# Kernel tuning notes

Measured on AMD Instinct MI355X. Metric: run time of the kernel, lower is better.

The kernel has to match this reference:

```python
import jax, jax.numpy as jnp
import numpy as np

H = 32          # heads
E = 32          # head dim = mdl_channels // heads (must equal heads per module bug)
C = 1024        # mdl_channels == in_channels
MAXP = 128      # max_position_embeddings
EPS = 1e-5


def _layernorm(x, g, b):
    mu = jnp.mean(x, axis=-1, keepdims=True)
    var = jnp.var(x, axis=-1, keepdims=True)
    return (x - mu) * jax.lax.rsqrt(var + EPS) * g + b


def setup_inputs() -> dict:
    key = jax.random.key(0)
    ks = jax.random.split(key, 16)
    s = 0.02
    N, L = 4, 1024
    inp = {
        "x": jax.random.normal(ks[0], (N, L, C), jnp.float32),
        "Wq": jax.random.normal(ks[1], (C, C), jnp.float32) * s,
        "bq": jnp.zeros((C,), jnp.float32),
        "Wk": jax.random.normal(ks[2], (C, C), jnp.float32) * s,
        "bk": jnp.zeros((C,), jnp.float32),
        "Wv": jax.random.normal(ks[3], (C, C), jnp.float32) * s,
        "bv": jnp.zeros((C,), jnp.float32),
        "dist_emb": jax.random.normal(ks[4], (2 * MAXP + 1, E), jnp.float32) * s,
        "ln1_g": jnp.ones((C,), jnp.float32),
        "ln1_b": jnp.zeros((C,), jnp.float32),
        "ln2_g": jnp.ones((C,), jnp.float32),
        "ln2_b": jnp.zeros((C,), jnp.float32),
        "W1": jax.random.normal(ks[5], (C, C), jnp.float32) * s,
        "b1": jnp.zeros((C,), jnp.float32),
        "W2": jax.random.normal(ks[6], (C, C), jnp.float32) * s,
        "b2": jnp.zeros((C,), jnp.float32),
    }
    return inp


def reference(x, Wq, bq, Wk, bk, Wv, bv, dist_emb, ln1_g, ln1_b,
              ln2_g, ln2_b, W1, b1, W2, b2):
    N, L, _ = x.shape
    # QKV projections -> (N, L, H, E)
    q = (x @ Wq + bq).reshape(N, L, H, E)
    k = (x @ Wk + bk).reshape(N, L, H, E)
    v = (x @ Wv + bv).reshape(N, L, H, E)

    temp = 1.0 / np.sqrt(E).astype(np.float32)
    # content scores (N, H, L, S)
    QK = jnp.einsum('nlhe,nshe->nhls', q, k)
    # relative position scores (disentangled attention)
    pos = jnp.arange(L)
    dist = jnp.clip(pos[:, None] - pos[None, :], -MAXP, MAXP) + MAXP  # (L, L)
    pe = dist_emb[dist]                                              # (L, L, E)
    QK = QK + jnp.einsum('nlhe,lse->nhls', q, pe) \
            + jnp.einsum('nshe,lse->nhls', k, pe)
    A = jax.nn.softmax(temp * QK, axis=-1)          # dropout: eval mode (identity)
    t = jnp.einsum('nhls,nshe->nlhe', A, v).reshape(N, L, C)

    h = _layernorm(t + x, ln1_g, ln1_b)             # AddNorm (attention)
    m = jax.nn.relu(h @ W1 + b1) @ W2 + b2          # 2-layer MLP
    out = _layernorm(m + h, ln2_g, ln2_b)           # AddNorm (mlp)
    return jnp.swapaxes(out, 0, 1)                  # 'n f c -> f n c'
```

## Files before the change

kernel.cpp:

```cpp
#include <hip/hip_runtime.h>

#define H_ 32
#define E_ 32
#define C_ 1024
#define L_ 1024
#define N_ 4
#define M_ 4096
#define NH_ 128
#define D_ 257
#define QDP 264
#define TEMP_ 0.17677669529663687f

typedef unsigned short u16;
typedef __attribute__((ext_vector_type(8))) short short8;
typedef __attribute__((ext_vector_type(4))) float f32x4;
typedef __attribute__((ext_vector_type(4))) unsigned short u16x4;

__device__ __forceinline__ u16 f2bf(float f) {
  union { float f; unsigned u; } v; v.f = f;
  unsigned r = v.u + 0x7fffu + ((v.u >> 16) & 1u);
  return (u16)(r >> 16);
}
__device__ __forceinline__ float bf2f(u16 h) {
  union { unsigned u; float f; } v; v.u = ((unsigned)h) << 16;
  return v.f;
}
__device__ __forceinline__ f32x4 mfma16(short8 a, short8 b, f32x4 c) {
  return __builtin_amdgcn_mfma_f32_16x16x32_bf16(a, b, c, 0, 0, 0);
}

__global__ __launch_bounds__(256) void prep_kernel(
    const float* __restrict__ demb, const float* __restrict__ bq,
    const float* __restrict__ bk, const float* __restrict__ bv,
    u16* __restrict__ demb_b, float* __restrict__ bqkv) {
  int i = blockIdx.x * 256 + threadIdx.x;
  if (i < D_ * E_) demb_b[i] = f2bf(demb[i]);
  if (i < C_) { bqkv[i] = bq[i]; bqkv[C_ + i] = bk[i]; bqkv[2 * C_ + i] = bv[i]; }
}

__global__ __launch_bounds__(256) void cvt_x_kernel(const float* __restrict__ x,
                                                    u16* __restrict__ xb) {
  int i = blockIdx.x * 256 + threadIdx.x;
  f32x4 v = reinterpret_cast<const f32x4*>(x)[i];
  u16x4 o2;
  o2[0] = f2bf(v[0]); o2[1] = f2bf(v[1]); o2[2] = f2bf(v[2]); o2[3] = f2bf(v[3]);
  reinterpret_cast<u16x4*>(xb)[i] = o2;
}

__global__ __launch_bounds__(256) void transpose_w_kernel(const float* __restrict__ in,
                                                          u16* __restrict__ out) {
  __shared__ float tile[32][33];
  int j0 = blockIdx.x * 32, c0 = blockIdx.y * 32;
#pragma unroll
  for (int i = 0; i < 4; ++i) {
    int cy = threadIdx.y + i * 8;
    tile[cy][threadIdx.x] = in[(size_t)(c0 + cy) * C_ + j0 + threadIdx.x];
  }
  __syncthreads();
#pragma unroll
  for (int i = 0; i < 4; ++i) {
    int jy = threadIdx.y + i * 8;
    out[(size_t)(j0 + jy) * C_ + c0 + threadIdx.x] = f2bf(tile[threadIdx.x][jy]);
  }
}

template <int EPI>
__global__ __launch_bounds__(256) void gemm128_kernel(
    const u16* __restrict__ A, const u16* __restrict__ Bt, int K,
    const float* __restrict__ bias,
    u16* __restrict__ out0, u16* __restrict__ out1, u16* __restrict__ out2) {
  __shared__ u16 As[128 * 64];
  __shared__ u16 Bs[128 * 64];
  const int bid = blockIdx.x;
  const int m0 = (bid & 31) << 7;
  const int n0 = (bid >> 5) << 7;
  const int tid = threadIdx.x;
  const int w = tid >> 6, lane = tid & 63, lhi = lane >> 4, llo = lane & 15;
  const int wr = w >> 1, wc = w & 1;
  f32x4 acc[4][4] = {};
  for (int k0 = 0; k0 < K; k0 += 64) {
#pragma unroll
    for (int i = 0; i < 4; ++i) {
      int e = i * 256 + tid;
      int row = e >> 3, c8 = (e & 7) << 3;
      *reinterpret_cast<short8*>(&As[row * 64 + c8]) =
          *reinterpret_cast<const short8*>(&A[(size_t)(m0 + row) * K + k0 + c8]);
      *reinterpret_cast<short8*>(&Bs[row * 64 + c8]) =
          *reinterpret_cast<const short8*>(&Bt[(size_t)(n0 + row) * K + k0 + c8]);
    }
    __syncthreads();
#pragma unroll
    for (int kk = 0; kk < 2; ++kk) {
      const int ko = (kk << 5) + lhi * 8;
      short8 af[4], bf[4];
#pragma unroll
      for (int mi = 0; mi < 4; ++mi)
        af[mi] = *reinterpret_cast<const short8*>(&As[(wr * 64 + mi * 16 + llo) * 64 + ko]);
#pragma unroll
      for (int ni = 0; ni < 4; ++ni)
        bf[ni] = *reinterpret_cast<const short8*>(&Bs[(wc * 64 + ni * 16 + llo) * 64 + ko]);
#pragma unroll
      for (int mi = 0; mi < 4; ++mi)
#pragma unroll
        for (int ni = 0; ni < 4; ++ni)
          acc[mi][ni] = mfma16(af[mi], bf[ni], acc[mi][ni]);
    }
    __syncthreads();
  }
#pragma unroll
  for (int mi = 0; mi < 4; ++mi)
#pragma unroll
    for (int ni = 0; ni < 4; ++ni)
#pragma unroll
      for (int r = 0; r < 4; ++r) {
        int row = m0 + wr * 64 + mi * 16 + lhi * 4 + r;
        int col = n0 + wc * 64 + ni * 16 + llo;
        float v = acc[mi][ni][r] + bias[col];
        if constexpr (EPI == 0) {
          int which = col >> 10, jj = col & 1023, h = jj >> 5, e2 = jj & 31;
          int n = row >> 10, l = row & 1023;
          int nh = (n << 5) | h;
          if (which == 0) v *= TEMP_;
          u16 bvv = f2bf(v);
          if (which == 0)      out0[((size_t)((nh << 10) | l)) * 32 + e2] = bvv;
          else if (which == 1) out1[((size_t)((nh << 10) | l)) * 32 + e2] = bvv;
          else                 out2[(((size_t)(nh * 32 + e2)) << 10) | l] = bvv;
        } else if constexpr (EPI == 1) {
          out0[(size_t)row * C_ + col] = f2bf(fmaxf(v, 0.f));
        } else {
          out0[(size_t)row * C_ + col] = f2bf(v);
        }
      }
}

__global__ __launch_bounds__(256) void qdkd_kernel(
    const u16* __restrict__ src, const u16* __restrict__ demb,
    u16* __restrict__ dst, int dstride, float scale,
    u16* __restrict__ aux0, u16* __restrict__ aux256) {
  const int wt = blockIdx.x * 4 + (threadIdx.x >> 6);
  const int lane = threadIdx.x & 63, lhi = lane >> 4, llo = lane & 15;
  const int m0 = wt << 4;
  short8 a = *reinterpret_cast<const short8*>(&src[(size_t)(m0 + llo) * E_ + lhi * 8]);
#pragma unroll
  for (int ct = 0; ct < 17; ++ct) {
    int d = ct * 16 + llo;
    short8 b = {0, 0, 0, 0, 0, 0, 0, 0};
    if (d < D_) b = *reinterpret_cast<const short8*>(&demb[d * E_ + lhi * 8]);
    f32x4 c = {};
    c = mfma16(a, b, c);
    if (d < D_) {
#pragma unroll
      for (int r = 0; r < 4; ++r) {
        u16 val = f2bf(c[r] * scale);
        dst[(size_t)(m0 + lhi * 4 + r) * dstride + d] = val;
        if (aux0 != nullptr && d == 0)     aux0[m0 + lhi * 4 + r] = val;
        if (aux256 != nullptr && d == 256) aux256[m0 + lhi * 4 + r] = val;
      }
    }
  }
}

__global__ __launch_bounds__(256) void attn_kernel(
    const u16* __restrict__ qw, const u16* __restrict__ kw,
    const u16* __restrict__ vT, const u16* __restrict__ QDg,
    const u16* __restrict__ KDg, const u16* __restrict__ kd0a,
    const u16* __restrict__ kd256a, u16* __restrict__ tb) {
  __shared__ u16 QDs[64 * QDP];
  __shared__ u16 kdc[2 * 1024];
  __shared__ u16 Pbuf[4 * 512];
  const int bid = blockIdx.x;
  const int nh = bid >> 4;
  const int l0 = (bid & 15) << 6;
  const int tid = threadIdx.x;
  const int w = tid >> 6, lane = tid & 63, lhi = lane >> 4, llo = lane & 15;
  const int lw0 = l0 + (w << 4);
  const int lg = lw0 + llo;
  const int lrow = (w << 4) + llo;

  const u16* qb  = qw + (size_t)nh * (L_ * E_);
  const u16* kb  = kw + (size_t)nh * (L_ * E_);
  const u16* vb  = vT + (size_t)nh * (E_ * L_);
  const u16* qdg = QDg + (size_t)nh * ((size_t)L_ * QDP);
  const u16* kdg = KDg + (size_t)nh * ((size_t)L_ * D_);

  {
    const int rr = tid >> 5, cc = tid & 31;
#pragma unroll
    for (int g = 0; g < 8; ++g) {
      int row = g * 8 + rr;
      *reinterpret_cast<short8*>(&QDs[row * QDP + cc * 8]) =
          *reinterpret_cast<const short8*>(&qdg[(size_t)(l0 + row) * QDP + cc * 8]);
    }
    if (tid < 64) QDs[tid * QDP + 256] = qdg[(size_t)(l0 + tid) * QDP + 256];
    const int side = tid >> 7, off = (tid & 127) * 8;
    const u16* srcA = (side ? kd256a : kd0a) + (size_t)nh * L_ + off;
    *reinterpret_cast<short8*>(&kdc[side * 1024 + off]) =
        *reinterpret_cast<const short8*>(srcA);
  }
  __syncthreads();

  const short8 qB = *reinterpret_cast<const short8*>(&qb[(size_t)lg * E_ + lhi * 8]);
  const float qd0   = bf2f(QDs[lrow * QDP + 0]);
  const float qd256 = bf2f(QDs[lrow * QDP + 256]);

  f32x4 o0 = {}, o1 = {};
  float l_acc = 0.f;
  char* Pw = reinterpret_cast<char*>(&Pbuf[w * 512]);

  for (int s0 = 0; s0 < L_; s0 += 32) {
    short8 kA0 = *reinterpret_cast<const short8*>(&kb[(size_t)(s0 + llo) * E_ + lhi * 8]);
    short8 kA1 = *reinterpret_cast<const short8*>(&kb[(size_t)(s0 + 16 + llo) * E_ + lhi * 8]);
    f32x4 st0 = {}, st1 = {};
    st0 = mfma16(kA0, qB, st0);
    st1 = mfma16(kA1, qB, st1);

    float p[8];
    const bool far_hi = (lw0 - (s0 + 31)) >= 128;
    const bool far_lo = (s0 - (lw0 + 15)) >= 128;
    if (far_hi || far_lo) {
      const float qdc = far_hi ? qd256 : qd0;
      const u16* kcb = &kdc[far_hi ? 1024 : 0];
      u16x4 kc0 = *reinterpret_cast<const u16x4*>(&kcb[s0 + lhi * 4]);
      u16x4 kc1 = *reinterpret_cast<const u16x4*>(&kcb[s0 + 16 + lhi * 4]);
#pragma unroll
      for (int r = 0; r < 4; ++r) {
        p[r]     = __expf(st0[r] + qdc + bf2f(kc0[r]));
        p[4 + r] = __expf(st1[r] + qdc + bf2f(kc1[r]));
      }
    } else {
#pragma unroll
      for (int i = 0; i < 2; ++i)
#pragma unroll
        for (int r = 0; r < 4; ++r) {
          const int scol = s0 + i * 16 + lhi * 4 + r;
          int d = lg - scol;
          d = (d < -128 ? -128 : (d > 128 ? 128 : d)) + 128;
          float qd = bf2f(QDs[lrow * QDP + d]);
          float kd = bf2f(kdg[(size_t)scol * D_ + d]);
          p[i * 4 + r] = __expf((i ? st1[r] : st0[r]) + qd + kd);
        }
    }
    l_acc += ((p[0] + p[1]) + (p[2] + p[3])) + ((p[4] + p[5]) + (p[6] + p[7]));

#pragma unroll
    for (int i = 0; i < 2; ++i)
#pragma unroll
      for (int b = 0; b < 2; ++b) {
        unsigned wv = (unsigned)f2bf(p[i * 4 + 2 * b]) |
                      ((unsigned)f2bf(p[i * 4 + 2 * b + 1]) << 16);
        int u = (i * 4 + lhi) ^ (llo & 6);
        *reinterpret_cast<unsigned*>(Pw + llo * 64 + u * 8 + b * 4) = wv;
      }
    short8 pB = *reinterpret_cast<const short8*>(
        Pw + llo * 64 + (((lhi * 2) ^ (llo & 6)) * 8));
    short8 vA0 = *reinterpret_cast<const short8*>(&vb[(size_t)llo * L_ + s0 + lhi * 8]);
    short8 vA1 = *reinterpret_cast<const short8*>(&vb[(size_t)(16 + llo) * L_ + s0 + lhi * 8]);
    o0 = mfma16(vA0, pB, o0);
    o1 = mfma16(vA1, pB, o1);
  }

  float l2 = l_acc + __shfl_xor(l_acc, 16);
  float lt = l2 + __shfl_xor(l2, 32);
  const float inv = 1.0f / lt;

  const int n = nh >> 5, h = nh & 31;
  const size_t obase = (((size_t)((n << 10) | lg)) * 32 + h) * 32;
  u16x4 w0, w1;
#pragma unroll
  for (int r = 0; r < 4; ++r) {
    w0[r] = f2bf(o0[r] * inv);
    w1[r] = f2bf(o1[r] * inv);
  }
  *reinterpret_cast<u16x4*>(&tb[obase + lhi * 4]) = w0;
  *reinterpret_cast<u16x4*>(&tb[obase + 16 + lhi * 4]) = w1;
}

__global__ __launch_bounds__(256) void ln1_kernel(
    const u16* __restrict__ tbuf, const float* __restrict__ x,
    const float* __restrict__ g, const float* __restrict__ b,
    u16* __restrict__ hb) {
  __shared__ float red[8];
  const int row = blockIdx.x, tid = threadIdx.x;
  const size_t base = (size_t)row * C_ + tid * 4;
  f32x4 xv = *reinterpret_cast<const f32x4*>(&x[base]);
  u16x4 tv = *reinterpret_cast<const u16x4*>(&tbuf[base]);
  float v[4]; float s1 = 0.f, s2 = 0.f;
#pragma unroll
  for (int i = 0; i < 4; ++i) {
    v[i] = xv[i] + bf2f(tv[i]);
    s1 += v[i]; s2 += v[i] * v[i];
  }
#pragma unroll
  for (int off = 32; off >= 1; off >>= 1) {
    s1 += __shfl_xor(s1, off); s2 += __shfl_xor(s2, off);
  }
  if ((tid & 63) == 0) { red[tid >> 6] = s1; red[4 + (tid >> 6)] = s2; }
  __syncthreads();
  float S1 = red[0] + red[1] + red[2] + red[3];
  float S2 = red[4] + red[5] + red[6] + red[7];
  float mu = S1 * (1.f / C_);
  float rs = rsqrtf(S2 * (1.f / C_) - mu * mu + 1e-5f);
#pragma unroll
  for (int i = 0; i < 4; ++i) {
    int c = tid * 4 + i;
    hb[base + i] = f2bf((v[i] - mu) * rs * g[c] + b[c]);
  }
}

__global__ __launch_bounds__(256) void ln2_kernel(
    const u16* __restrict__ mb, const u16* __restrict__ hb,
    const float* __restrict__ g, const float* __restrict__ b,
    float* __restrict__ out) {
  __shared__ float red[8];
  const int row = blockIdx.x, tid = threadIdx.x;
  const size_t base = (size_t)row * C_ + tid * 4;
  u16x4 mv = *reinterpret_cast<const u16x4*>(&mb[base]);
  u16x4 hv = *reinterpret_cast<const u16x4*>(&hb[base]);
  float v[4]; float s1 = 0.f, s2 = 0.f;
#pragma unroll
  for (int i = 0; i < 4; ++i) {
    v[i] = bf2f(mv[i]) + bf2f(hv[i]);
    s1 += v[i]; s2 += v[i] * v[i];
  }
#pragma unroll
  for (int off = 32; off >= 1; off >>= 1) {
    s1 += __shfl_xor(s1, off); s2 += __shfl_xor(s2, off);
  }
  if ((tid & 63) == 0) { red[tid >> 6] = s1; red[4 + (tid >> 6)] = s2; }
  __syncthreads();
  float S1 = red[0] + red[1] + red[2] + red[3];
  float S2 = red[4] + red[5] + red[6] + red[7];
  float mu = S1 * (1.f / C_);
  float rs = rsqrtf(S2 * (1.f / C_) - mu * mu + 1e-5f);
  const int n = row >> 10, l = row & 1023;
  const size_t ob = (size_t)(l * N_ + n) * C_ + tid * 4;
#pragma unroll
  for (int i = 0; i < 4; ++i) {
    int c = tid * 4 + i;
    out[ob + i] = (v[i] - mu) * rs * g[c] + b[c];
  }
}

extern "C" void kernel_launch(void* const* d_in, const int* in_sizes, int n_in,
                              void* d_out, int out_size, void* d_ws, size_t ws_size,
                              hipStream_t stream) {
  const float* x    = (const float*)d_in[0];
  const float* Wq   = (const float*)d_in[1];
  const float* bq   = (const float*)d_in[2];
  const float* Wk   = (const float*)d_in[3];
  const float* bk   = (const float*)d_in[4];
  const float* Wv   = (const float*)d_in[5];
  const float* bv   = (const float*)d_in[6];
  const float* demb = (const float*)d_in[7];
  const float* g1   = (const float*)d_in[8];
  const float* b1ln = (const float*)d_in[9];
  const float* g2   = (const float*)d_in[10];
  const float* b2ln = (const float*)d_in[11];
  const float* W1   = (const float*)d_in[12];
  const float* b1   = (const float*)d_in[13];
  const float* W2   = (const float*)d_in[14];
  const float* b2   = (const float*)d_in[15];
  float* outp = (float*)d_out;

  size_t o = 0;
  auto alloc = [&](size_t bytes) { size_t r = o; o += (bytes + 255) & ~(size_t)255; return r; };
  const size_t xb_o    = alloc((size_t)M_ * C_ * 2);
  const size_t wqkv_o  = alloc((size_t)3 * C_ * C_ * 2);
  const size_t w1_o    = alloc((size_t)C_ * C_ * 2);
  const size_t w2_o    = alloc((size_t)C_ * C_ * 2);
  const size_t bqkv_o  = alloc((size_t)3 * C_ * 4);
  const size_t demb_o  = alloc((size_t)D_ * E_ * 2);
  const size_t q_o     = alloc((size_t)NH_ * L_ * E_ * 2);
  const size_t k_o     = alloc((size_t)NH_ * L_ * E_ * 2);
  const size_t vt_o    = alloc((size_t)NH_ * L_ * E_ * 2);
  const size_t qd_o    = alloc((size_t)NH_ * L_ * QDP * 2);
  const size_t kd_o    = alloc((size_t)NH_ * L_ * D_ * 2);
  const size_t kd0_o   = alloc((size_t)NH_ * L_ * 2);
  const size_t kd256_o = alloc((size_t)NH_ * L_ * 2);
  const size_t t_o     = alloc((size_t)M_ * C_ * 2);
  const size_t h_o     = alloc((size_t)M_ * C_ * 2);
  const size_t m1_o    = alloc((size_t)M_ * C_ * 2);
  const size_t m_o     = alloc((size_t)M_ * C_ * 2);
  if (o > ws_size) return;

  char* ws = (char*)d_ws;
  u16*   xb     = (u16*)(ws + xb_o);
  u16*   wqkv_t = (u16*)(ws + wqkv_o);
  u16*   w1_t   = (u16*)(ws + w1_o);
  u16*   w2_t   = (u16*)(ws + w2_o);
  float* bqkv   = (float*)(ws + bqkv_o);
  u16*   demb_b = (u16*)(ws + demb_o);
  u16*   q_ws   = (u16*)(ws + q_o);
  u16*   k_ws   = (u16*)(ws + k_o);
  u16*   vT_ws  = (u16*)(ws + vt_o);
  u16*   QD     = (u16*)(ws + qd_o);
  u16*   KD     = (u16*)(ws + kd_o);
  u16*   kd0a   = (u16*)(ws + kd0_o);
  u16*   kd256a = (u16*)(ws + kd256_o);
  u16*   t_b16  = (u16*)(ws + t_o);
  u16*   h_b16  = (u16*)(ws + h_o);
  u16*   m1_b16 = (u16*)(ws + m1_o);
  u16*   m_b16  = (u16*)(ws + m_o);

  prep_kernel<<<33, 256, 0, stream>>>(demb, bq, bk, bv, demb_b, bqkv);
  cvt_x_kernel<<<(M_ * C_) / 1024, 256, 0, stream>>>(x, xb);
  dim3 tb_(32, 8), tg_(32, 32);
  transpose_w_kernel<<<tg_, tb_, 0, stream>>>(Wq, wqkv_t);
  transpose_w_kernel<<<tg_, tb_, 0, stream>>>(Wk, wqkv_t + (size_t)C_ * C_);
  transpose_w_kernel<<<tg_, tb_, 0, stream>>>(Wv, wqkv_t + (size_t)2 * C_ * C_);
  transpose_w_kernel<<<tg_, tb_, 0, stream>>>(W1, w1_t);
  transpose_w_kernel<<<tg_, tb_, 0, stream>>>(W2, w2_t);

  gemm128_kernel<0><<<32 * 24, 256, 0, stream>>>(xb, wqkv_t, C_, bqkv, q_ws, k_ws, vT_ws);

  qdkd_kernel<<<2048, 256, 0, stream>>>(q_ws, demb_b, QD, QDP, 1.0f, nullptr, nullptr);
  qdkd_kernel<<<2048, 256, 0, stream>>>(k_ws, demb_b, KD, D_, TEMP_, kd0a, kd256a);

  attn_kernel<<<NH_ * 16, 256, 0, stream>>>(q_ws, k_ws, vT_ws, QD, KD, kd0a, kd256a, t_b16);

  ln1_kernel<<<M_, 256, 0, stream>>>(t_b16, x, g1, b1ln, h_b16);

  gemm128_kernel<1><<<32 * 8, 256, 0, stream>>>(h_b16, w1_t, C_, b1, m1_b16, nullptr, nullptr);
  gemm128_kernel<2><<<32 * 8, 256, 0, stream>>>(m1_b16, w2_t, C_, b2, m_b16, nullptr, nullptr);

  ln2_kernel<<<M_, 256, 0, stream>>>(m_b16, h_b16, g2, b2ln, outp);
}
```

Measured before the change: 308.9 us.

## Restructure attention score tiles, fold log2e into scales, use direct-to-LDS GEMM loads

The attention kernel now computes scores as Q·K^T so each lane holds four query rows for one key column. It adds a fast path for tiles entirely inside the relative-distance band, which reads contiguous 4-wide vectors of the key-distance table using its 257-stride diagonal structure. The log2(e) factor is folded into the q and key-distance scaling so the exponential can be a raw v_exp_f32, and the P buffer uses a padded layout with simpler bf16 packing. The GEMM tile loads go straight from global memory into LDS via global_load_lds, skipping the register round trip. These changes add more complex indexing and row-sum reduction logic, and there is a risk of LDS bank conflicts or mistakes in the handling of band edges.

```diff
diff --git a/kernel.cpp b/kernel.cpp
--- a/kernel.cpp
+++ b/kernel.cpp
@@ -10,6 +10,7 @@
 #define D_ 257
 #define QDP 264
 #define TEMP_ 0.17677669529663687f
+#define QSCALE_ (TEMP_ * 1.4426950408889634f)
 
 typedef unsigned short u16;
 typedef __attribute__((ext_vector_type(8))) short short8;
@@ -27,6 +28,16 @@
 }
 __device__ __forceinline__ f32x4 mfma16(short8 a, short8 b, f32x4 c) {
   return __builtin_amdgcn_mfma_f32_16x16x32_bf16(a, b, c, 0, 0, 0);
+}
+__device__ __forceinline__ float exp2a(float x) {
+  float r;
+  asm("v_exp_f32 %0, %1\n\ts_nop 1" : "=v"(r) : "v"(x));
+  return r;
+}
+__device__ __forceinline__ void gld16(const u16* g, u16* l) {
+  __builtin_amdgcn_global_load_lds(
+      (const __attribute__((address_space(1))) unsigned int*)g,
+      (__attribute__((address_space(3))) unsigned int*)l, 16, 0, 0);
 }
 
 __global__ __launch_bounds__(256) void prep_kernel(
@@ -77,16 +88,16 @@
   const int tid = threadIdx.x;
   const int w = tid >> 6, lane = tid & 63, lhi = lane >> 4, llo = lane & 15;
   const int wr = w >> 1, wc = w & 1;
+  const int w4 = w << 2;
+  const int srow = lane >> 3, scol = (lane & 7) << 3;
   f32x4 acc[4][4] = {};
   for (int k0 = 0; k0 < K; k0 += 64) {
 #pragma unroll
-    for (int i = 0; i < 4; ++i) {
-      int e = i * 256 + tid;
-      int row = e >> 3, c8 = (e & 7) << 3;
-      *reinterpret_cast<short8*>(&As[row * 64 + c8]) =
-          *reinterpret_cast<const short8*>(&A[(size_t)(m0 + row) * K + k0 + c8]);
-      *reinterpret_cast<short8*>(&Bs[row * 64 + c8]) =
-          *reinterpret_cast<const short8*>(&Bt[(size_t)(n0 + row) * K + k0 + c8]);
+    for (int j = 0; j < 4; ++j) {
+      const int seg = w4 + j;
+      const int row = (seg << 3) + srow;
+      gld16(&A[(size_t)(m0 + row) * K + k0 + scol], &As[seg << 9]);
+      gld16(&Bt[(size_t)(n0 + row) * K + k0 + scol], &Bs[seg << 9]);
     }
     __syncthreads();
 #pragma unroll
@@ -120,7 +131,7 @@
           int which = col >> 10, jj = col & 1023, h = jj >> 5, e2 = jj & 31;
           int n = row >> 10, l = row & 1023;
           int nh = (n << 5) | h;
-          if (which == 0) v *= TEMP_;
+          if (which == 0) v *= QSCALE_;
           u16 bvv = f2bf(v);
           if (which == 0)      out0[((size_t)((nh << 10) | l)) * 32 + e2] = bvv;
           else if (which == 1) out1[((size_t)((nh << 10) | l)) * 32 + e2] = bvv;
@@ -167,15 +178,14 @@
     const u16* __restrict__ kd256a, u16* __restrict__ tb) {
   __shared__ u16 QDs[64 * QDP];
   __shared__ u16 kdc[2 * 1024];
-  __shared__ u16 Pbuf[4 * 512];
+  __shared__ u16 Pbuf[4 * 16 * 40];
+  __shared__ float Lred[64];
   const int bid = blockIdx.x;
   const int nh = bid >> 4;
   const int l0 = (bid & 15) << 6;
   const int tid = threadIdx.x;
   const int w = tid >> 6, lane = tid & 63, lhi = lane >> 4, llo = lane & 15;
   const int lw0 = l0 + (w << 4);
-  const int lg = lw0 + llo;
-  const int lrow = (w << 4) + llo;
 
   const u16* qb  = qw + (size_t)nh * (L_ * E_);
   const u16* kb  = kw + (size_t)nh * (L_ * E_);
@@ -184,14 +194,14 @@
   const u16* kdg = KDg + (size_t)nh * ((size_t)L_ * D_);
 
   {
-    const int rr = tid >> 5, cc = tid & 31;
-#pragma unroll
-    for (int g = 0; g < 8; ++g) {
-      int row = g * 8 + rr;
-      *reinterpret_cast<short8*>(&QDs[row * QDP + cc * 8]) =
-          *reinterpret_cast<const short8*>(&qdg[(size_t)(l0 + row) * QDP + cc * 8]);
-    }
-    if (tid < 64) QDs[tid * QDP + 256] = qdg[(size_t)(l0 + tid) * QDP + 256];
+    const int rr = tid >> 2, q4 = tid & 3;
+#pragma unroll
+    for (int j = 0; j < 9; ++j) {
+      int c = q4 + j * 4;
+      if (c < 33)
+        *reinterpret_cast<short8*>(&QDs[rr * QDP + c * 8]) =
+            *reinterpret_cast<const short8*>(&qdg[(size_t)(l0 + rr) * QDP + c * 8]);
+    }
     const int side = tid >> 7, off = (tid & 127) * 8;
     const u16* srcA = (side ? kd256a : kd0a) + (size_t)nh * L_ + off;
     *reinterpret_cast<short8*>(&kdc[side * 1024 + off]) =
@@ -199,80 +209,101 @@
   }
   __syncthreads();
 
-  const short8 qB = *reinterpret_cast<const short8*>(&qb[(size_t)lg * E_ + lhi * 8]);
-  const float qd0   = bf2f(QDs[lrow * QDP + 0]);
-  const float qd256 = bf2f(QDs[lrow * QDP + 256]);
-
+  const short8 qA = *reinterpret_cast<const short8*>(&qb[(size_t)(lw0 + llo) * E_ + lhi * 8]);
+  const int qr4 = (w << 4) + (lhi << 2);
+  float qdf0[4], qdf256[4];
+#pragma unroll
+  for (int r = 0; r < 4; ++r) {
+    qdf0[r]   = bf2f(QDs[(qr4 + r) * QDP + 0]);
+    qdf256[r] = bf2f(QDs[(qr4 + r) * QDP + 256]);
+  }
+
+  u16* Pw = &Pbuf[w * 16 * 40];
   f32x4 o0 = {}, o1 = {};
-  float l_acc = 0.f;
-  char* Pw = reinterpret_cast<char*>(&Pbuf[w * 512]);
+  float lacc[4] = {0.f, 0.f, 0.f, 0.f};
 
   for (int s0 = 0; s0 < L_; s0 += 32) {
-    short8 kA0 = *reinterpret_cast<const short8*>(&kb[(size_t)(s0 + llo) * E_ + lhi * 8]);
-    short8 kA1 = *reinterpret_cast<const short8*>(&kb[(size_t)(s0 + 16 + llo) * E_ + lhi * 8]);
+    short8 kB0 = *reinterpret_cast<const short8*>(&kb[(size_t)(s0 + llo) * E_ + lhi * 8]);
+    short8 kB1 = *reinterpret_cast<const short8*>(&kb[(size_t)(s0 + 16 + llo) * E_ + lhi * 8]);
     f32x4 st0 = {}, st1 = {};
-    st0 = mfma16(kA0, qB, st0);
-    st1 = mfma16(kA1, qB, st1);
-
-    float p[8];
-    const bool far_hi = (lw0 - (s0 + 31)) >= 128;
-    const bool far_lo = (s0 - (lw0 + 15)) >= 128;
-    if (far_hi || far_lo) {
-      const float qdc = far_hi ? qd256 : qd0;
-      const u16* kcb = &kdc[far_hi ? 1024 : 0];
-      u16x4 kc0 = *reinterpret_cast<const u16x4*>(&kcb[s0 + lhi * 4]);
-      u16x4 kc1 = *reinterpret_cast<const u16x4*>(&kcb[s0 + 16 + lhi * 4]);
+    st0 = mfma16(qA, kB0, st0);
+    st1 = mfma16(qA, kB1, st1);
+
+    const int dmin = lw0 - s0 - 31, dmax = lw0 + 15 - s0;
+    float p0[4], p1[4];
+    if (dmin >= 128 || dmax <= -128) {
+      const int sd = (dmin >= 128) ? 1 : 0;
+      const float* qdf = sd ? qdf256 : qdf0;
+      const float kc0 = bf2f(kdc[sd * 1024 + s0 + llo]);
+      const float kc1 = bf2f(kdc[sd * 1024 + s0 + 16 + llo]);
 #pragma unroll
       for (int r = 0; r < 4; ++r) {
-        p[r]     = __expf(st0[r] + qdc + bf2f(kc0[r]));
-        p[4 + r] = __expf(st1[r] + qdc + bf2f(kc1[r]));
+        p0[r] = exp2a(st0[r] + qdf[r] + kc0);
+        p1[r] = exp2a(st1[r] + qdf[r] + kc1);
+      }
+    } else if (dmin >= -128 && dmax <= 128) {
+      const int sc0 = s0 + llo, sc1 = s0 + 16 + llo;
+      u16x4 kd0v = *reinterpret_cast<const u16x4*>(&kdg[256 * sc0 + lw0 + (lhi << 2) + 128]);
+      u16x4 kd1v = *reinterpret_cast<const u16x4*>(&kdg[256 * sc1 + lw0 + (lhi << 2) + 128]);
+#pragma unroll
+      for (int r = 0; r < 4; ++r) {
+        const int qq = lw0 + (lhi << 2) + r;
+        float qd0 = bf2f(QDs[(qr4 + r) * QDP + (qq - sc0 + 128)]);
+        float qd1 = bf2f(QDs[(qr4 + r) * QDP + (qq - sc1 + 128)]);
+        p0[r] = exp2a(st0[r] + qd0 + bf2f(kd0v[r]));
+        p1[r] = exp2a(st1[r] + qd1 + bf2f(kd1v[r]));
       }
     } else {
 #pragma unroll
-      for (int i = 0; i < 2; ++i)
-#pragma unroll
-        for (int r = 0; r < 4; ++r) {
-          const int scol = s0 + i * 16 + lhi * 4 + r;
-          int d = lg - scol;
-          d = (d < -128 ? -128 : (d > 128 ? 128 : d)) + 128;
-          float qd = bf2f(QDs[lrow * QDP + d]);
-          float kd = bf2f(kdg[(size_t)scol * D_ + d]);
-          p[i * 4 + r] = __expf((i ? st1[r] : st0[r]) + qd + kd);
-        }
-    }
-    l_acc += ((p[0] + p[1]) + (p[2] + p[3])) + ((p[4] + p[5]) + (p[6] + p[7]));
-
-#pragma unroll
-    for (int i = 0; i < 2; ++i)
-#pragma unroll
-      for (int b = 0; b < 2; ++b) {
-        unsigned wv = (unsigned)f2bf(p[i * 4 + 2 * b]) |
-                      ((unsigned)f2bf(p[i * 4 + 2 * b + 1]) << 16);
-        int u = (i * 4 + lhi) ^ (llo & 6);
-        *reinterpret_cast<unsigned*>(Pw + llo * 64 + u * 8 + b * 4) = wv;
+      for (int r = 0; r < 4; ++r) {
+        const int qq = lw0 + (lhi << 2) + r;
+        int d0 = qq - (s0 + llo);
+        d0 = (d0 < -128 ? -128 : (d0 > 128 ? 128 : d0)) + 128;
+        int d1 = qq - (s0 + 16 + llo);
+        d1 = (d1 < -128 ? -128 : (d1 > 128 ? 128 : d1)) + 128;
+        float qd0 = bf2f(QDs[(qr4 + r) * QDP + d0]);
+        float qd1 = bf2f(QDs[(qr4 + r) * QDP + d1]);
+        float kd0 = bf2f(kdg[(size_t)(s0 + llo) * D_ + d0]);
+        float kd1 = bf2f(kdg[(size_t)(s0 + 16 + llo) * D_ + d1]);
+        p0[r] = exp2a(st0[r] + qd0 + kd0);
+        p1[r] = exp2a(st1[r] + qd1 + kd1);
       }
-    short8 pB = *reinterpret_cast<const short8*>(
-        Pw + llo * 64 + (((lhi * 2) ^ (llo & 6)) * 8));
+    }
+
+#pragma unroll
+    for (int r = 0; r < 4; ++r) {
+      lacc[r] += p0[r] + p1[r];
+      union { float f; unsigned u; } a0, a1; a0.f = p0[r]; a1.f = p1[r];
+      const int prow = ((lhi << 2) + r) * 40;
+      Pw[prow + llo]      = (u16)((a0.u + 0x8000u) >> 16);
+      Pw[prow + 16 + llo] = (u16)((a1.u + 0x8000u) >> 16);
+    }
+    short8 pB = *reinterpret_cast<const short8*>(&Pw[llo * 40 + lhi * 8]);
     short8 vA0 = *reinterpret_cast<const short8*>(&vb[(size_t)llo * L_ + s0 + lhi * 8]);
     short8 vA1 = *reinterpret_cast<const short8*>(&vb[(size_t)(16 + llo) * L_ + s0 + lhi * 8]);
     o0 = mfma16(vA0, pB, o0);
     o1 = mfma16(vA1, pB, o1);
   }
 
-  float l2 = l_acc + __shfl_xor(l_acc, 16);
-  float lt = l2 + __shfl_xor(l2, 32);
-  const float inv = 1.0f / lt;
+#pragma unroll
+  for (int r = 0; r < 4; ++r) {
+    float t = lacc[r];
+    t += __shfl_xor(t, 1); t += __shfl_xor(t, 2);
+    t += __shfl_xor(t, 4); t += __shfl_xor(t, 8);
+    if (llo == 0) Lred[(w << 4) + (lhi << 2) + r] = t;
+  }
+  const float inv = 1.0f / Lred[(w << 4) + llo];
 
   const int n = nh >> 5, h = nh & 31;
-  const size_t obase = (((size_t)((n << 10) | lg)) * 32 + h) * 32;
+  const size_t obase = (((size_t)((n << 10) | (lw0 + llo))) * 32 + h) * 32;
   u16x4 w0, w1;
 #pragma unroll
   for (int r = 0; r < 4; ++r) {
     w0[r] = f2bf(o0[r] * inv);
     w1[r] = f2bf(o1[r] * inv);
   }
-  *reinterpret_cast<u16x4*>(&tb[obase + lhi * 4]) = w0;
-  *reinterpret_cast<u16x4*>(&tb[obase + 16 + lhi * 4]) = w1;
+  *reinterpret_cast<u16x4*>(&tb[obase + (lhi << 2)]) = w0;
+  *reinterpret_cast<u16x4*>(&tb[obase + 16 + (lhi << 2)]) = w1;
 }
 
 __global__ __launch_bounds__(256) void ln1_kernel(
@@ -414,7 +445,7 @@
   gemm128_kernel<0><<<32 * 24, 256, 0, stream>>>(xb, wqkv_t, C_, bqkv, q_ws, k_ws, vT_ws);
 
   qdkd_kernel<<<2048, 256, 0, stream>>>(q_ws, demb_b, QD, QDP, 1.0f, nullptr, nullptr);
-  qdkd_kernel<<<2048, 256, 0, stream>>>(k_ws, demb_b, KD, D_, TEMP_, kd0a, kd256a);
+  qdkd_kernel<<<2048, 256, 0, stream>>>(k_ws, demb_b, KD, D_, QSCALE_, kd0a, kd256a);
 
   attn_kernel<<<NH_ * 16, 256, 0, stream>>>(q_ws, k_ws, vT_ws, QD, KD, kd0a, kd256a, t_b16);
 
```

Result: slower. 321.7 us (+4.2%).
